# Kernel tuning notes

Hardware: AMD Instinct MI355X
Metric: run time of the kernel (lower is better)

Reference implementation:

```python
import jax, jax.numpy as jnp
import numpy as np

HEAD_DIM = 128
NUM_HEADS = 16
GROUP_SIZE = 8


def setup_inputs() -> dict:
    key = jax.random.key(0)
    k1, k2, k3 = jax.random.split(key, 3)
    B, T, K = 2, 2048, 2048
    query = jax.random.normal(k1, (B, T, NUM_HEADS * HEAD_DIM), dtype=jnp.float32)
    k_ = jax.random.normal(k2, (B, K, NUM_HEADS, HEAD_DIM), dtype=jnp.float32)
    v_ = jax.random.normal(k3, (B, K, NUM_HEADS, HEAD_DIM), dtype=jnp.float32)
    return {"query": query, "key": k_, "value": v_}


def reference(query, key, value):
    B, T, _ = query.shape
    g = GROUP_SIZE
    # (B, T//g, g, H, D)
    gq = query.reshape(B, T // g, g, NUM_HEADS, HEAD_DIM)
    scale = jnp.sqrt(jnp.asarray(HEAD_DIM, dtype=query.dtype))
    # scores: (B, T//g, g, H, K)
    scores = jnp.einsum('btghd,bkhd->btghk', gq, key) / scale
    attention = jax.nn.softmax(scores, axis=-1)
    out = jnp.einsum('btghk,bkhd->btghd', attention, value)
    return out.reshape(B, T, -1)
```

## Files before the change

### kernel.cpp

```cpp
#include <hip/hip_runtime.h>


#define T_   2048
#define KLEN 2048
#define H_   16
#define D_   128
#define BH_  32
#define NT_  (KLEN / 64)

typedef unsigned short u16;
typedef short bf16x8 __attribute__((ext_vector_type(8), may_alias));
typedef float f32x4 __attribute__((ext_vector_type(4)));
typedef float f32x8 __attribute__((ext_vector_type(8), may_alias));
typedef unsigned int u32a __attribute__((may_alias));
typedef u16 u16a __attribute__((may_alias));

__device__ __forceinline__ u16 f2bf(float f) {
    unsigned int u = __builtin_bit_cast(unsigned int, f);
    u += 0x7fffu + ((u >> 16) & 1u);
    return (u16)(u >> 16);
}
__device__ __forceinline__ unsigned int pk2(float a, float b) {
    unsigned int r;
    asm("v_cvt_pk_bf16_f32 %0, %1, %2" : "=v"(r) : "v"(a), "v"(b));
    return r;
}

__device__ __forceinline__ void async_cp16(const void* g, void* l) {
    __builtin_amdgcn_global_load_lds(
        (const __attribute__((address_space(1))) unsigned int*)g,
        (__attribute__((address_space(3))) unsigned int*)l, 16, 0, 0);
}

#define FR_ELEMS ((size_t)KLEN * D_)
#define WS_NEED  (2 * BH_ * FR_ELEMS * sizeof(u16))
#define PW_BYTES 2304
#define SM_BUF   32768
#define SM_TOTAL (2 * SM_BUF + 4 * PW_BYTES)

__global__ __launch_bounds__(256)
void prep_fused(const float* __restrict__ k_g, const float* __restrict__ v_g,
                u16* __restrict__ kf, u16* __restrict__ vf) {
    __shared__ __align__(16) unsigned char sm[16384];
    if (blockIdx.x < 4096) {
        const int id   = blockIdx.x * 256 + threadIdx.x;
        const int lane = id & 63;
        const int dc   = (id >> 6) & 3;
        const int kb   = (id >> 8) & 127;
        const int bh   = id >> 15;
        const int b = bh >> 4, h = bh & 15;
        const int c = lane & 15, quad = lane >> 4;
        const float* src = k_g + ((size_t)(b * KLEN + kb * 16 + c) * H_ + h) * D_
                               + dc * 32 + quad * 8;
        f32x8 v = *(const f32x8*)src;
        uint4 w;
        w.x = pk2(v[0], v[1]); w.y = pk2(v[2], v[3]);
        w.z = pk2(v[4], v[5]); w.w = pk2(v[6], v[7]);
        *(uint4*)(kf + (size_t)id * 8) = w;
    } else {
        const int bid  = blockIdx.x - 4096;
        const int kt64 = bid & 31;
        const int bh   = bid >> 5;
        const int b = bh >> 4, h = bh & 15;
        const float* vbase = v_g + ((size_t)b * KLEN * H_ + h) * D_;
        const int sc0 = threadIdx.x & 15;
        const int spr = threadIdx.x >> 4;
        #pragma unroll
        for (int rr = 0; rr < 2; ++rr) {
            const int r0 = 2 * (spr + 16 * rr);
            const float* vp = vbase + (size_t)(kt64 * 64 + r0) * (H_ * D_) + sc0 * 8;
            f32x8 va = *(const f32x8*)vp;
            f32x8 vb = *(const f32x8*)(vp + H_ * D_);
            const int g_hi = r0 >> 3;
            const int woff = (r0 & 7) * 2;
            #pragma unroll
            for (int j = 0; j < 8; ++j) {
                const int d = sc0 * 8 + j;
                const int g = g_hi ^ ((d ^ (d >> 3)) & 7);
                *(u32a*)(sm + d * 128 + g * 16 + woff) = pk2(va[j], vb[j]);
            }
        }
        __syncthreads();
        u16* obase = vf + (size_t)bh * FR_ELEMS;
        #pragma unroll
        for (int i = 0; i < 4; ++i) {
            const int gid  = threadIdx.x + 256 * i;
            const int lane = gid & 63;
            const int dt   = (gid >> 6) & 7;
            const int kgl  = gid >> 9;
            const int c = lane & 15, quad = lane >> 4;
            const int d  = dt * 16 + c;
            const int kl = kgl * 32 + quad * 8;
            const int g  = (kl >> 3) ^ ((d ^ (d >> 3)) & 7);
            uint4 w = *(const uint4*)(sm + d * 128 + g * 16);
            const int kg = kt64 * 2 + kgl;
            *(uint4*)(obase + ((size_t)(kg * 8 + dt) * 64 + lane) * 8) = w;
        }
    }
}


__global__ __launch_bounds__(256, 2)
void gqa_fa4(const float* __restrict__ q_g, const u16* __restrict__ kf,
             const u16* __restrict__ vf, float* __restrict__ o_g) {
    __shared__ __align__(16) unsigned char smem[SM_TOTAL];

    const int lane = threadIdx.x & 63;
    const int wave = threadIdx.x >> 6;
    const int c    = lane & 15;
    const int quad = lane >> 4;

    const int blk = blockIdx.x;
    const int bh  = (blk & 7) * 4 + (blk >> 8);
    const int qt  = (blk >> 3) & 31;
    const int b   = bh >> 4, h = bh & 15;

    const int q0 = qt * 64 + wave * 16;

    bf16x8 qf[4];
    {
        const float* qbase = q_g + (size_t)(b * T_ + q0 + c) * (H_ * D_) + h * D_ + quad * 8;
        #pragma unroll
        for (int dc = 0; dc < 4; ++dc) {
            f32x8 qv = *(const f32x8*)(qbase + dc * 32);
            uint4 w;
            w.x = pk2(qv[0], qv[1]); w.y = pk2(qv[2], qv[3]);
            w.z = pk2(qv[4], qv[5]); w.w = pk2(qv[6], qv[7]);
            qf[dc] = __builtin_bit_cast(bf16x8, w);
        }
    }

    const u16* KFb = kf + (size_t)bh * FR_ELEMS;
    const u16* VFb = vf + (size_t)bh * FR_ELEMS;

    f32x4 acc_o[8];
    #pragma unroll
    for (int dt = 0; dt < 8; ++dt) acc_o[dt] = (f32x4){0.f, 0.f, 0.f, 0.f};
    float l_i[4] = {0.f, 0.f, 0.f, 0.f};

    const float kexp = 0.12751744f;
    unsigned char* Pw = smem + 2 * SM_BUF + wave * PW_BYTES;

    auto stage = [&](int buf, int kt) {
        const u16* ksrc = KFb + (size_t)kt * 8192;
        const u16* vsrc = VFb + (size_t)kt * 8192;
        unsigned char* base = smem + buf * SM_BUF;
        #pragma unroll
        for (int j = 0; j < 8; ++j) {
            const int idx = wave * 8 + j;
            if (idx < 16)
                async_cp16(ksrc + idx * 512 + lane * 8, base + idx * 1024);
            else
                async_cp16(vsrc + (idx - 16) * 512 + lane * 8,
                           base + 16384 + (idx - 16) * 1024);
        }
    };

    stage(0, 0);
    __syncthreads();

    for (int kt = 0; kt < NT_; ++kt) {
        const int cur = kt & 1;
        if (kt + 1 < NT_) stage(cur ^ 1, kt + 1);

        const unsigned char* kbuf = smem + cur * SM_BUF;
        const unsigned char* vbuf = kbuf + 16384;

        f32x4 s[4];
        __builtin_amdgcn_s_setprio(1);
        #pragma unroll
        for (int nt = 0; nt < 4; ++nt) {
            s[nt] = (f32x4){0.f, 0.f, 0.f, 0.f};
            #pragma unroll
            for (int dc = 0; dc < 4; ++dc) {
                bf16x8 kfr = *(const bf16x8*)(kbuf + (nt * 4 + dc) * 1024 + lane * 16);
                s[nt] = __builtin_amdgcn_mfma_f32_16x16x32_bf16(qf[dc], kfr, s[nt], 0, 0, 0);
            }
        }
        __builtin_amdgcn_s_setprio(0);

        #pragma unroll
        for (int r = 0; r < 4; ++r) {
            const float p0 = exp2f(s[0][r] * kexp);
            const float p1 = exp2f(s[1][r] * kexp);
            const float p2 = exp2f(s[2][r] * kexp);
            const float p3 = exp2f(s[3][r] * kexp);
            l_i[r] += (p0 + p1) + (p2 + p3);
            const unsigned int u01 = pk2(p0, p1);
            const unsigned int u23 = pk2(p2, p3);
            u16a* row = (u16a*)(Pw + (quad * 4 + r) * 144);
            row[c]      = (u16)u01;
            row[16 + c] = (u16)(u01 >> 16);
            row[32 + c] = (u16)u23;
            row[48 + c] = (u16)(u23 >> 16);
        }

        __builtin_amdgcn_s_setprio(1);
        #pragma unroll
        for (int kc = 0; kc < 2; ++kc) {
            bf16x8 pf = *(const bf16x8*)(Pw + (c * 72 + kc * 32 + quad * 8) * 2);
            #pragma unroll
            for (int dt = 0; dt < 8; ++dt) {
                bf16x8 vfr = *(const bf16x8*)(vbuf + (kc * 8 + dt) * 1024 + lane * 16);
                acc_o[dt] = __builtin_amdgcn_mfma_f32_16x16x32_bf16(pf, vfr, acc_o[dt], 0, 0, 0);
            }
        }
        __builtin_amdgcn_s_setprio(0);

        __syncthreads();
    }

    #pragma unroll
    for (int r = 0; r < 4; ++r) {
        float t = l_i[r];
        t += __shfl_xor(t, 1);
        t += __shfl_xor(t, 2);
        t += __shfl_xor(t, 4);
        t += __shfl_xor(t, 8);
        const float inv = 1.f / t;
        const int qrow = q0 + quad * 4 + r;
        float* op = o_g + (size_t)(b * T_ + qrow) * (H_ * D_) + h * D_ + c;
        #pragma unroll
        for (int dt = 0; dt < 8; ++dt)
            op[dt * 16] = acc_o[dt][r] * inv;
    }
}


#define VT_BYTES 16384
#define KT_BYTES (64 * 136 * 2)

__global__ __launch_bounds__(256, 2)
void gqa_fa_v1(const float* __restrict__ q_g, const float* __restrict__ k_g,
               const float* __restrict__ v_g, float* __restrict__ o_g) {
    __shared__ __align__(16) unsigned char smem[VT_BYTES + KT_BYTES + 4 * PW_BYTES];
    unsigned char* VtB = smem;
    unsigned char* KtB = smem + VT_BYTES;
    const int lane = threadIdx.x & 63;
    const int wave = threadIdx.x >> 6;
    const int c    = lane & 15;
    const int quad = lane >> 4;
    const int qt = blockIdx.x & 31;
    const int bh = blockIdx.x >> 5;
    const int h  = bh & 15;
    const int b  = bh >> 4;
    const int q0 = qt * 64 + wave * 16;
    bf16x8 qf[4];
    {
        const float* qbase = q_g + (size_t)(b * T_ + q0 + c) * (H_ * D_) + h * D_ + quad * 8;
        #pragma unroll
        for (int dc = 0; dc < 4; ++dc) {
            f32x8 qv = *(const f32x8*)(qbase + dc * 32);
            uint4 w;
            w.x = pk2(qv[0], qv[1]); w.y = pk2(qv[2], qv[3]);
            w.z = pk2(qv[4], qv[5]); w.w = pk2(qv[6], qv[7]);
            qf[dc] = __builtin_bit_cast(bf16x8, w);
        }
    }
    f32x4 acc_o[8];
    #pragma unroll
    for (int dt = 0; dt < 8; ++dt) acc_o[dt] = (f32x4){0.f, 0.f, 0.f, 0.f};
    float m_i[4], l_i[4];
    #pragma unroll
    for (int r = 0; r < 4; ++r) { m_i[r] = -1e30f; l_i[r] = 0.f; }
    const float kexp = 0.12751744f;
    unsigned char* Pw = smem + VT_BYTES + KT_BYTES + wave * PW_BYTES;
    const int sc0 = threadIdx.x & 15;
    const int spr = threadIdx.x >> 4;
    const size_t kvstride = (size_t)(H_ * D_);
    const float* kbase = k_g + ((size_t)b * KLEN * H_ + h) * D_;
    const float* vbase = v_g + ((size_t)b * KLEN * H_ + h) * D_;
    for (int kt = 0; kt < KLEN / 64; ++kt) {
        __syncthreads();
        #pragma unroll
        for (int i = 0; i < 4; ++i) {
            const int id   = threadIdx.x + 256 * i;
            const int row  = id >> 4;
            const int dcol = (id & 15) * 8;
            const float* kp = kbase + (size_t)(kt * 64 + row) * kvstride + dcol;
            f32x8 kv = *(const f32x8*)kp;
            uint4 w;
            w.x = pk2(kv[0], kv[1]); w.y = pk2(kv[2], kv[3]);
            w.z = pk2(kv[4], kv[5]); w.w = pk2(kv[6], kv[7]);
            *(uint4*)(KtB + (row * 136 + dcol) * 2) = w;
        }
        #pragma unroll
        for (int rr = 0; rr < 2; ++rr) {
            const int r0 = 2 * (spr + 16 * rr);
            const float* vp = vbase + (size_t)(kt * 64 + r0) * kvstride + sc0 * 8;
            f32x8 va = *(const f32x8*)vp;
            f32x8 vb = *(const f32x8*)(vp + kvstride);
            const int g_hi = r0 >> 3;
            const int woff = (r0 & 7) * 2;
            #pragma unroll
            for (int j = 0; j < 8; ++j) {
                const int d = sc0 * 8 + j;
                const int g = g_hi ^ ((d ^ (d >> 3)) & 7);
                *(u32a*)(VtB + d * 128 + g * 16 + woff) = pk2(va[j], vb[j]);
            }
        }
        __syncthreads();
        f32x4 s[4];
        #pragma unroll
        for (int nt = 0; nt < 4; ++nt) {
            s[nt] = (f32x4){0.f, 0.f, 0.f, 0.f};
            const u16* kfp = (const u16*)KtB + (nt * 16 + c) * 136 + quad * 8;
            #pragma unroll
            for (int dc = 0; dc < 4; ++dc) {
                bf16x8 kfr = *(const bf16x8*)(kfp + dc * 32);
                s[nt] = __builtin_amdgcn_mfma_f32_16x16x32_bf16(qf[dc], kfr, s[nt], 0, 0, 0);
            }
        }
        #pragma unroll
        for (int r = 0; r < 4; ++r) {
            float v = fmaxf(fmaxf(s[0][r], s[1][r]), fmaxf(s[2][r], s[3][r]));
            v = fmaxf(v, __shfl_xor(v, 1));
            v = fmaxf(v, __shfl_xor(v, 2));
            v = fmaxf(v, __shfl_xor(v, 4));
            v = fmaxf(v, __shfl_xor(v, 8));
            const float mnew  = fmaxf(m_i[r], v);
            const float alpha = exp2f((m_i[r] - mnew) * kexp);
            m_i[r] = mnew;
            l_i[r] *= alpha;
            #pragma unroll
            for (int dt = 0; dt < 8; ++dt) acc_o[dt][r] *= alpha;
            float sum = 0.f;
            #pragma unroll
            for (int nt = 0; nt < 4; ++nt) {
                const float p = exp2f((s[nt][r] - mnew) * kexp);
                sum += p;
                *(u16a*)(Pw + ((quad * 4 + r) * 72 + nt * 16 + c) * 2) = f2bf(p);
            }
            float t = sum;
            t += __shfl_xor(t, 1);
            t += __shfl_xor(t, 2);
            t += __shfl_xor(t, 4);
            t += __shfl_xor(t, 8);
            l_i[r] += t;
        }
        __syncthreads();
        #pragma unroll
        for (int kc = 0; kc < 2; ++kc) {
            bf16x8 pf = *(const bf16x8*)(Pw + (c * 72 + kc * 32 + quad * 8) * 2);
            const int k0 = kc * 32 + quad * 8;
            #pragma unroll
            for (int dt = 0; dt < 8; ++dt) {
                const int d = dt * 16 + c;
                const int g = (k0 >> 3) ^ ((d ^ (d >> 3)) & 7);
                bf16x8 vfr = *(const bf16x8*)(VtB + d * 128 + g * 16);
                acc_o[dt] = __builtin_amdgcn_mfma_f32_16x16x32_bf16(pf, vfr, acc_o[dt], 0, 0, 0);
            }
        }
    }
    #pragma unroll
    for (int r = 0; r < 4; ++r) {
        const float inv = 1.f / l_i[r];
        const int qrow = q0 + quad * 4 + r;
        float* op = o_g + (size_t)(b * T_ + qrow) * (H_ * D_) + h * D_ + c;
        #pragma unroll
        for (int dt = 0; dt < 8; ++dt)
            op[dt * 16] = acc_o[dt][r] * inv;
    }
}

extern "C" void kernel_launch(void* const* d_in, const int* in_sizes, int n_in,
                              void* d_out, int out_size, void* d_ws, size_t ws_size,
                              hipStream_t stream) {
    const float* q = (const float*)d_in[0];
    const float* k = (const float*)d_in[1];
    const float* v = (const float*)d_in[2];
    float* o = (float*)d_out;
    if (ws_size >= WS_NEED) {
        u16* kfb = (u16*)d_ws;
        u16* vfb = kfb + (size_t)BH_ * FR_ELEMS;
        prep_fused<<<dim3(5120), dim3(256), 0, stream>>>(k, v, kfb, vfb);
        gqa_fa4<<<dim3(1024), dim3(256), 0, stream>>>(q, kfb, vfb, o);
    } else {
        gqa_fa_v1<<<dim3(1024), dim3(256), 0, stream>>>(q, k, v, o);
    }
}
```

Measured before the change: 237.2 us.

## Process two 16-row query tiles per wave to reuse K/V fragments

Each wave now handles 32 query rows (two MFMA M-tiles) instead of 16. Every K and V fragment read from LDS feeds two MFMAs, and each block covers 128 queries, so the grid is halved and K/V staging traffic per query drops by half. The P scratch buffer is enlarged and given an XOR swizzle to avoid LDS bank conflicts. The cost is more accumulator registers per wave, a larger LDS footprint, and only 512 blocks, which may limit occupancy and wave-level parallelism.

```diff
diff --git a/kernel.cpp b/kernel.cpp
--- a/kernel.cpp
+++ b/kernel.cpp
@@ -34,8 +34,8 @@
 
 #define FR_ELEMS ((size_t)KLEN * D_)
 #define WS_NEED  (2 * BH_ * FR_ELEMS * sizeof(u16))
-#define PW_BYTES 2304
 #define SM_BUF   32768
+#define PW_BYTES 4096
 #define SM_TOTAL (2 * SM_BUF + 4 * PW_BYTES)
 
 __global__ __launch_bounds__(256)
@@ -111,32 +111,36 @@
     const int quad = lane >> 4;
 
     const int blk = blockIdx.x;
-    const int bh  = (blk & 7) * 4 + (blk >> 8);
-    const int qt  = (blk >> 3) & 31;
+    const int bh  = (blk & 7) * 4 + (blk >> 7);
+    const int qt  = (blk >> 3) & 15;
     const int b   = bh >> 4, h = bh & 15;
 
-    const int q0 = qt * 64 + wave * 16;
-
-    bf16x8 qf[4];
-    {
-        const float* qbase = q_g + (size_t)(b * T_ + q0 + c) * (H_ * D_) + h * D_ + quad * 8;
+    const int q0 = qt * 128 + wave * 32;
+
+    bf16x8 qf[2][4];
+    #pragma unroll
+    for (int mt = 0; mt < 2; ++mt) {
+        const float* qbase = q_g + (size_t)(b * T_ + q0 + mt * 16 + c) * (H_ * D_)
+                                 + h * D_ + quad * 8;
         #pragma unroll
         for (int dc = 0; dc < 4; ++dc) {
             f32x8 qv = *(const f32x8*)(qbase + dc * 32);
             uint4 w;
             w.x = pk2(qv[0], qv[1]); w.y = pk2(qv[2], qv[3]);
             w.z = pk2(qv[4], qv[5]); w.w = pk2(qv[6], qv[7]);
-            qf[dc] = __builtin_bit_cast(bf16x8, w);
+            qf[mt][dc] = __builtin_bit_cast(bf16x8, w);
         }
     }
 
     const u16* KFb = kf + (size_t)bh * FR_ELEMS;
     const u16* VFb = vf + (size_t)bh * FR_ELEMS;
 
-    f32x4 acc_o[8];
-    #pragma unroll
-    for (int dt = 0; dt < 8; ++dt) acc_o[dt] = (f32x4){0.f, 0.f, 0.f, 0.f};
-    float l_i[4] = {0.f, 0.f, 0.f, 0.f};
+    f32x4 acc_o[2][8];
+    #pragma unroll
+    for (int mt = 0; mt < 2; ++mt)
+        #pragma unroll
+        for (int dt = 0; dt < 8; ++dt) acc_o[mt][dt] = (f32x4){0.f, 0.f, 0.f, 0.f};
+    float l_i[2][4] = {{0.f, 0.f, 0.f, 0.f}, {0.f, 0.f, 0.f, 0.f}};
 
     const float kexp = 0.12751744f;
     unsigned char* Pw = smem + 2 * SM_BUF + wave * PW_BYTES;
@@ -166,43 +170,56 @@
         const unsigned char* kbuf = smem + cur * SM_BUF;
         const unsigned char* vbuf = kbuf + 16384;
 
-        f32x4 s[4];
+        f32x4 s0[4], s1[4];
         __builtin_amdgcn_s_setprio(1);
         #pragma unroll
         for (int nt = 0; nt < 4; ++nt) {
-            s[nt] = (f32x4){0.f, 0.f, 0.f, 0.f};
+            s0[nt] = (f32x4){0.f, 0.f, 0.f, 0.f};
+            s1[nt] = (f32x4){0.f, 0.f, 0.f, 0.f};
             #pragma unroll
             for (int dc = 0; dc < 4; ++dc) {
                 bf16x8 kfr = *(const bf16x8*)(kbuf + (nt * 4 + dc) * 1024 + lane * 16);
-                s[nt] = __builtin_amdgcn_mfma_f32_16x16x32_bf16(qf[dc], kfr, s[nt], 0, 0, 0);
+                s0[nt] = __builtin_amdgcn_mfma_f32_16x16x32_bf16(qf[0][dc], kfr, s0[nt], 0, 0, 0);
+                s1[nt] = __builtin_amdgcn_mfma_f32_16x16x32_bf16(qf[1][dc], kfr, s1[nt], 0, 0, 0);
             }
         }
         __builtin_amdgcn_s_setprio(0);
 
         #pragma unroll
-        for (int r = 0; r < 4; ++r) {
-            const float p0 = exp2f(s[0][r] * kexp);
-            const float p1 = exp2f(s[1][r] * kexp);
-            const float p2 = exp2f(s[2][r] * kexp);
-            const float p3 = exp2f(s[3][r] * kexp);
-            l_i[r] += (p0 + p1) + (p2 + p3);
-            const unsigned int u01 = pk2(p0, p1);
-            const unsigned int u23 = pk2(p2, p3);
-            u16a* row = (u16a*)(Pw + (quad * 4 + r) * 144);
-            row[c]      = (u16)u01;
-            row[16 + c] = (u16)(u01 >> 16);
-            row[32 + c] = (u16)u23;
-            row[48 + c] = (u16)(u23 >> 16);
+        for (int mt = 0; mt < 2; ++mt) {
+            #pragma unroll
+            for (int r = 0; r < 4; ++r) {
+                const f32x4* s = mt ? s1 : s0;
+                const float p0 = exp2f(s[0][r] * kexp);
+                const float p1 = exp2f(s[1][r] * kexp);
+                const float p2 = exp2f(s[2][r] * kexp);
+                const float p3 = exp2f(s[3][r] * kexp);
+                l_i[mt][r] += (p0 + p1) + (p2 + p3);
+                const unsigned int u01 = pk2(p0, p1);
+                const unsigned int u23 = pk2(p2, p3);
+                const int prow = mt * 16 + quad * 4 + r;
+                unsigned char* row = Pw + prow * 128;
+                const int swz = (prow & 7) << 4;
+                *(u16a*)(row + ((2 * c) ^ swz))      = (u16)u01;
+                *(u16a*)(row + ((32 + 2 * c) ^ swz)) = (u16)(u01 >> 16);
+                *(u16a*)(row + ((64 + 2 * c) ^ swz)) = (u16)u23;
+                *(u16a*)(row + ((96 + 2 * c) ^ swz)) = (u16)(u23 >> 16);
+            }
         }
 
         __builtin_amdgcn_s_setprio(1);
         #pragma unroll
         for (int kc = 0; kc < 2; ++kc) {
-            bf16x8 pf = *(const bf16x8*)(Pw + (c * 72 + kc * 32 + quad * 8) * 2);
+            const int pr0 = c;
+            const int pr1 = 16 + c;
+            const int off = (kc * 64 + quad * 16) ^ ((c & 7) << 4);
+            bf16x8 pf0 = *(const bf16x8*)(Pw + pr0 * 128 + off);
+            bf16x8 pf1 = *(const bf16x8*)(Pw + pr1 * 128 + off);
             #pragma unroll
             for (int dt = 0; dt < 8; ++dt) {
                 bf16x8 vfr = *(const bf16x8*)(vbuf + (kc * 8 + dt) * 1024 + lane * 16);
-                acc_o[dt] = __builtin_amdgcn_mfma_f32_16x16x32_bf16(pf, vfr, acc_o[dt], 0, 0, 0);
+                acc_o[0][dt] = __builtin_amdgcn_mfma_f32_16x16x32_bf16(pf0, vfr, acc_o[0][dt], 0, 0, 0);
+                acc_o[1][dt] = __builtin_amdgcn_mfma_f32_16x16x32_bf16(pf1, vfr, acc_o[1][dt], 0, 0, 0);
             }
         }
         __builtin_amdgcn_s_setprio(0);
@@ -211,29 +228,33 @@
     }
 
     #pragma unroll
-    for (int r = 0; r < 4; ++r) {
-        float t = l_i[r];
-        t += __shfl_xor(t, 1);
-        t += __shfl_xor(t, 2);
-        t += __shfl_xor(t, 4);
-        t += __shfl_xor(t, 8);
-        const float inv = 1.f / t;
-        const int qrow = q0 + quad * 4 + r;
-        float* op = o_g + (size_t)(b * T_ + qrow) * (H_ * D_) + h * D_ + c;
-        #pragma unroll
-        for (int dt = 0; dt < 8; ++dt)
-            op[dt * 16] = acc_o[dt][r] * inv;
+    for (int mt = 0; mt < 2; ++mt) {
+        #pragma unroll
+        for (int r = 0; r < 4; ++r) {
+            float t = l_i[mt][r];
+            t += __shfl_xor(t, 1);
+            t += __shfl_xor(t, 2);
+            t += __shfl_xor(t, 4);
+            t += __shfl_xor(t, 8);
+            const float inv = 1.f / t;
+            const int qrow = q0 + mt * 16 + quad * 4 + r;
+            float* op = o_g + (size_t)(b * T_ + qrow) * (H_ * D_) + h * D_ + c;
+            #pragma unroll
+            for (int dt = 0; dt < 8; ++dt)
+                op[dt * 16] = acc_o[mt][dt][r] * inv;
+        }
     }
 }
 
 
 #define VT_BYTES 16384
 #define KT_BYTES (64 * 136 * 2)
+#define PWF_BYTES 2304
 
 __global__ __launch_bounds__(256, 2)
 void gqa_fa_v1(const float* __restrict__ q_g, const float* __restrict__ k_g,
                const float* __restrict__ v_g, float* __restrict__ o_g) {
-    __shared__ __align__(16) unsigned char smem[VT_BYTES + KT_BYTES + 4 * PW_BYTES];
+    __shared__ __align__(16) unsigned char smem[VT_BYTES + KT_BYTES + 4 * PWF_BYTES];
     unsigned char* VtB = smem;
     unsigned char* KtB = smem + VT_BYTES;
     const int lane = threadIdx.x & 63;
@@ -264,7 +285,7 @@
     #pragma unroll
     for (int r = 0; r < 4; ++r) { m_i[r] = -1e30f; l_i[r] = 0.f; }
     const float kexp = 0.12751744f;
-    unsigned char* Pw = smem + VT_BYTES + KT_BYTES + wave * PW_BYTES;
+    unsigned char* Pw = smem + VT_BYTES + KT_BYTES + wave * PWF_BYTES;
     const int sc0 = threadIdx.x & 15;
     const int spr = threadIdx.x >> 4;
     const size_t kvstride = (size_t)(H_ * D_);
@@ -374,7 +395,7 @@
         u16* kfb = (u16*)d_ws;
         u16* vfb = kfb + (size_t)BH_ * FR_ELEMS;
         prep_fused<<<dim3(5120), dim3(256), 0, stream>>>(k, v, kfb, vfb);
-        gqa_fa4<<<dim3(1024), dim3(256), 0, stream>>>(q, kfb, vfb, o);
+        gqa_fa4<<<dim3(512), dim3(256), 0, stream>>>(q, kfb, vfb, o);
     } else {
         gqa_fa_v1<<<dim3(1024), dim3(256), 0, stream>>>(q, k, v, o);
     }
```

Measured after the change: 222.0 us. 6.4% less time.

## Switch attention to 32x32x16 MFMA with register-resident P via permlane swap

Applied to the files above, without the earlier changes.

Rewrites the fast attention kernel to use 32x32x16 bf16 MFMAs with 8 waves of 32 query rows each (256 queries per block), and changes the K/V pre-pack layout in the prep kernel to match the new fragment shapes. S is computed transposed (K as A operand), so the softmax probabilities can be repacked into the PV A-operand in registers using v_permlane32_swap instead of a round trip through LDS. The goal is fewer LDS writes and reads, fewer MFMA issues, and more reuse of each K/V tile across queries. In exchange it raises register pressure (f32x16 accumulators, 8 Q fragments) and launches only 256 blocks, which may leave some compute units underused.

```diff
diff --git a/kernel.cpp b/kernel.cpp
--- a/kernel.cpp
+++ b/kernel.cpp
@@ -12,6 +12,7 @@
 typedef short bf16x8 __attribute__((ext_vector_type(8), may_alias));
 typedef float f32x4 __attribute__((ext_vector_type(4)));
 typedef float f32x8 __attribute__((ext_vector_type(8), may_alias));
+typedef float f32x16 __attribute__((ext_vector_type(16)));
 typedef unsigned int u32a __attribute__((may_alias));
 typedef u16 u16a __attribute__((may_alias));
 
@@ -25,6 +26,9 @@
     asm("v_cvt_pk_bf16_f32 %0, %1, %2" : "=v"(r) : "v"(a), "v"(b));
     return r;
 }
+__device__ __forceinline__ void pl_swap(unsigned int& a, unsigned int& b) {
+    asm("v_permlane32_swap_b32 %0, %1" : "+v"(a), "+v"(b));
+}
 
 __device__ __forceinline__ void async_cp16(const void* g, void* l) {
     __builtin_amdgcn_global_load_lds(
@@ -34,24 +38,23 @@
 
 #define FR_ELEMS ((size_t)KLEN * D_)
 #define WS_NEED  (2 * BH_ * FR_ELEMS * sizeof(u16))
-#define PW_BYTES 2304
 #define SM_BUF   32768
-#define SM_TOTAL (2 * SM_BUF + 4 * PW_BYTES)
 
 __global__ __launch_bounds__(256)
 void prep_fused(const float* __restrict__ k_g, const float* __restrict__ v_g,
                 u16* __restrict__ kf, u16* __restrict__ vf) {
     __shared__ __align__(16) unsigned char sm[16384];
     if (blockIdx.x < 4096) {
-        const int id   = blockIdx.x * 256 + threadIdx.x;
-        const int lane = id & 63;
-        const int dc   = (id >> 6) & 3;
-        const int kb   = (id >> 8) & 127;
-        const int bh   = id >> 15;
+        const int id     = blockIdx.x * 256 + threadIdx.x;
+        const int lane   = id & 63;
+        const int dchunk = (id >> 6) & 7;
+        const int ktile  = (id >> 9) & 1;
+        const int kt64   = (id >> 10) & 31;
+        const int bh     = id >> 15;
         const int b = bh >> 4, h = bh & 15;
-        const int c = lane & 15, quad = lane >> 4;
-        const float* src = k_g + ((size_t)(b * KLEN + kb * 16 + c) * H_ + h) * D_
-                               + dc * 32 + quad * 8;
+        const int key = kt64 * 64 + ktile * 32 + (lane & 31);
+        const int d0  = dchunk * 16 + (lane >> 5) * 8;
+        const float* src = k_g + ((size_t)(b * KLEN + key) * H_ + h) * D_ + d0;
         f32x8 v = *(const f32x8*)src;
         uint4 w;
         w.x = pk2(v[0], v[1]); w.y = pk2(v[2], v[3]);
@@ -84,70 +87,87 @@
         u16* obase = vf + (size_t)bh * FR_ELEMS;
         #pragma unroll
         for (int i = 0; i < 4; ++i) {
-            const int gid  = threadIdx.x + 256 * i;
-            const int lane = gid & 63;
-            const int dt   = (gid >> 6) & 7;
-            const int kgl  = gid >> 9;
-            const int c = lane & 15, quad = lane >> 4;
-            const int d  = dt * 16 + c;
-            const int kl = kgl * 32 + quad * 8;
-            const int g  = (kl >> 3) ^ ((d ^ (d >> 3)) & 7);
+            const int gid   = threadIdx.x + 256 * i;
+            const int lane  = gid & 63;
+            const int ntile = (gid >> 6) & 3;
+            const int kc    = (gid >> 8) & 3;
+            const int key0  = kc * 16 + (lane >> 5) * 8;
+            const int d     = ntile * 32 + (lane & 31);
+            const int g     = (key0 >> 3) ^ ((d ^ (d >> 3)) & 7);
             uint4 w = *(const uint4*)(sm + d * 128 + g * 16);
-            const int kg = kt64 * 2 + kgl;
-            *(uint4*)(obase + ((size_t)(kg * 8 + dt) * 64 + lane) * 8) = w;
-        }
-    }
-}
-
-
-__global__ __launch_bounds__(256, 2)
-void gqa_fa4(const float* __restrict__ q_g, const u16* __restrict__ kf,
+            *(uint4*)(obase + ((size_t)(kt64 * 16 + kc * 4 + ntile) * 64 + lane) * 8) = w;
+        }
+    }
+}
+
+
+struct PA2 { bf16x8 f0, f1; };
+
+__device__ __forceinline__ PA2 softmax_pack(f32x16 st, float kexp, float& lacc) {
+    float p[16];
+    #pragma unroll
+    for (int r = 0; r < 16; ++r) p[r] = exp2f(st[r] * kexp);
+    lacc += (((p[0] + p[1]) + (p[2] + p[3])) + ((p[4] + p[5]) + (p[6] + p[7])))
+          + (((p[8] + p[9]) + (p[10] + p[11])) + ((p[12] + p[13]) + (p[14] + p[15])));
+    unsigned int a0 = pk2(p[0], p[1]),   b0 = pk2(p[4], p[5]);
+    unsigned int a1 = pk2(p[2], p[3]),   b1 = pk2(p[6], p[7]);
+    unsigned int a2 = pk2(p[8], p[9]),   b2 = pk2(p[12], p[13]);
+    unsigned int a3 = pk2(p[10], p[11]), b3 = pk2(p[14], p[15]);
+    pl_swap(a0, b0); pl_swap(a1, b1); pl_swap(a2, b2); pl_swap(a3, b3);
+    uint4 w0; w0.x = a0; w0.y = a1; w0.z = b0; w0.w = b1;
+    uint4 w1; w1.x = a2; w1.y = a3; w1.z = b2; w1.w = b3;
+    PA2 r;
+    r.f0 = __builtin_bit_cast(bf16x8, w0);
+    r.f1 = __builtin_bit_cast(bf16x8, w1);
+    return r;
+}
+
+__global__ __launch_bounds__(512, 2)
+void gqa_fa5(const float* __restrict__ q_g, const u16* __restrict__ kf,
              const u16* __restrict__ vf, float* __restrict__ o_g) {
-    __shared__ __align__(16) unsigned char smem[SM_TOTAL];
+    __shared__ __align__(16) unsigned char smem[2 * SM_BUF];
 
     const int lane = threadIdx.x & 63;
     const int wave = threadIdx.x >> 6;
-    const int c    = lane & 15;
-    const int quad = lane >> 4;
+    const int half = lane >> 5;
+    const int col  = lane & 31;
 
     const int blk = blockIdx.x;
-    const int bh  = (blk & 7) * 4 + (blk >> 8);
-    const int qt  = (blk >> 3) & 31;
-    const int b   = bh >> 4, h = bh & 15;
-
-    const int q0 = qt * 64 + wave * 16;
-
-    bf16x8 qf[4];
+    const int bh  = (blk & 7) * 4 + (blk >> 6);
+    const int qt  = (blk >> 3) & 7;
+    const int b = bh >> 4, h = bh & 15;
+
+    const int q0 = qt * 256 + wave * 32;
+
+    bf16x8 qf[8];
     {
-        const float* qbase = q_g + (size_t)(b * T_ + q0 + c) * (H_ * D_) + h * D_ + quad * 8;
-        #pragma unroll
-        for (int dc = 0; dc < 4; ++dc) {
-            f32x8 qv = *(const f32x8*)(qbase + dc * 32);
+        const float* qbase = q_g + (size_t)(b * T_ + q0 + col) * (H_ * D_)
+                                 + h * D_ + half * 8;
+        #pragma unroll
+        for (int dchunk = 0; dchunk < 8; ++dchunk) {
+            f32x8 qv = *(const f32x8*)(qbase + dchunk * 16);
             uint4 w;
             w.x = pk2(qv[0], qv[1]); w.y = pk2(qv[2], qv[3]);
             w.z = pk2(qv[4], qv[5]); w.w = pk2(qv[6], qv[7]);
-            qf[dc] = __builtin_bit_cast(bf16x8, w);
+            qf[dchunk] = __builtin_bit_cast(bf16x8, w);
         }
     }
 
     const u16* KFb = kf + (size_t)bh * FR_ELEMS;
     const u16* VFb = vf + (size_t)bh * FR_ELEMS;
 
-    f32x4 acc_o[8];
-    #pragma unroll
-    for (int dt = 0; dt < 8; ++dt) acc_o[dt] = (f32x4){0.f, 0.f, 0.f, 0.f};
-    float l_i[4] = {0.f, 0.f, 0.f, 0.f};
+    f32x16 acc[4] = {};
+    float l_part = 0.f;
 
     const float kexp = 0.12751744f;
-    unsigned char* Pw = smem + 2 * SM_BUF + wave * PW_BYTES;
 
     auto stage = [&](int buf, int kt) {
         const u16* ksrc = KFb + (size_t)kt * 8192;
         const u16* vsrc = VFb + (size_t)kt * 8192;
         unsigned char* base = smem + buf * SM_BUF;
         #pragma unroll
-        for (int j = 0; j < 8; ++j) {
-            const int idx = wave * 8 + j;
+        for (int j = 0; j < 4; ++j) {
+            const int idx = wave * 4 + j;
             if (idx < 16)
                 async_cp16(ksrc + idx * 512 + lane * 8, base + idx * 1024);
             else
@@ -166,43 +186,31 @@
         const unsigned char* kbuf = smem + cur * SM_BUF;
         const unsigned char* vbuf = kbuf + 16384;
 
-        f32x4 s[4];
+        f32x16 s0 = {}, s1 = {};
         __builtin_amdgcn_s_setprio(1);
         #pragma unroll
-        for (int nt = 0; nt < 4; ++nt) {
-            s[nt] = (f32x4){0.f, 0.f, 0.f, 0.f};
-            #pragma unroll
-            for (int dc = 0; dc < 4; ++dc) {
-                bf16x8 kfr = *(const bf16x8*)(kbuf + (nt * 4 + dc) * 1024 + lane * 16);
-                s[nt] = __builtin_amdgcn_mfma_f32_16x16x32_bf16(qf[dc], kfr, s[nt], 0, 0, 0);
-            }
+        for (int dchunk = 0; dchunk < 8; ++dchunk) {
+            bf16x8 kfr0 = *(const bf16x8*)(kbuf + dchunk * 1024 + lane * 16);
+            bf16x8 kfr1 = *(const bf16x8*)(kbuf + (8 + dchunk) * 1024 + lane * 16);
+            s0 = __builtin_amdgcn_mfma_f32_32x32x16_bf16(kfr0, qf[dchunk], s0, 0, 0, 0);
+            s1 = __builtin_amdgcn_mfma_f32_32x32x16_bf16(kfr1, qf[dchunk], s1, 0, 0, 0);
         }
         __builtin_amdgcn_s_setprio(0);
 
-        #pragma unroll
-        for (int r = 0; r < 4; ++r) {
-            const float p0 = exp2f(s[0][r] * kexp);
-            const float p1 = exp2f(s[1][r] * kexp);
-            const float p2 = exp2f(s[2][r] * kexp);
-            const float p3 = exp2f(s[3][r] * kexp);
-            l_i[r] += (p0 + p1) + (p2 + p3);
-            const unsigned int u01 = pk2(p0, p1);
-            const unsigned int u23 = pk2(p2, p3);
-            u16a* row = (u16a*)(Pw + (quad * 4 + r) * 144);
-            row[c]      = (u16)u01;
-            row[16 + c] = (u16)(u01 >> 16);
-            row[32 + c] = (u16)u23;
-            row[48 + c] = (u16)(u23 >> 16);
-        }
-
+        PA2 pa01 = softmax_pack(s0, kexp, l_part);
+        PA2 pa23 = softmax_pack(s1, kexp, l_part);
+
+        bf16x8 pfrag0 = pa01.f0, pfrag1 = pa01.f1;
+        bf16x8 pfrag2 = pa23.f0, pfrag3 = pa23.f1;
         __builtin_amdgcn_s_setprio(1);
         #pragma unroll
-        for (int kc = 0; kc < 2; ++kc) {
-            bf16x8 pf = *(const bf16x8*)(Pw + (c * 72 + kc * 32 + quad * 8) * 2);
-            #pragma unroll
-            for (int dt = 0; dt < 8; ++dt) {
-                bf16x8 vfr = *(const bf16x8*)(vbuf + (kc * 8 + dt) * 1024 + lane * 16);
-                acc_o[dt] = __builtin_amdgcn_mfma_f32_16x16x32_bf16(pf, vfr, acc_o[dt], 0, 0, 0);
+        for (int kc = 0; kc < 4; ++kc) {
+            const bf16x8 paf = (kc == 0) ? pfrag0 : (kc == 1) ? pfrag1
+                             : (kc == 2) ? pfrag2 : pfrag3;
+            #pragma unroll
+            for (int nt2 = 0; nt2 < 4; ++nt2) {
+                bf16x8 vfr = *(const bf16x8*)(vbuf + (kc * 4 + nt2) * 1024 + lane * 16);
+                acc[nt2] = __builtin_amdgcn_mfma_f32_32x32x16_bf16(paf, vfr, acc[nt2], 0, 0, 0);
             }
         }
         __builtin_amdgcn_s_setprio(0);
@@ -210,30 +218,30 @@
         __syncthreads();
     }
 
-    #pragma unroll
-    for (int r = 0; r < 4; ++r) {
-        float t = l_i[r];
-        t += __shfl_xor(t, 1);
-        t += __shfl_xor(t, 2);
-        t += __shfl_xor(t, 4);
-        t += __shfl_xor(t, 8);
-        const float inv = 1.f / t;
-        const int qrow = q0 + quad * 4 + r;
-        float* op = o_g + (size_t)(b * T_ + qrow) * (H_ * D_) + h * D_ + c;
-        #pragma unroll
-        for (int dt = 0; dt < 8; ++dt)
-            op[dt * 16] = acc_o[dt][r] * inv;
+    const float l_full = l_part + __shfl_xor(l_part, 32);
+    float* lds_l = (float*)smem;
+    if (half == 0) lds_l[wave * 32 + col] = 1.f / l_full;
+    __syncthreads();
+    #pragma unroll
+    for (int r = 0; r < 16; ++r) {
+        const int qrow = (r & 3) + 8 * (r >> 2) + 4 * half;
+        const float inv = lds_l[wave * 32 + qrow];
+        float* op = o_g + (size_t)(b * T_ + q0 + qrow) * (H_ * D_) + h * D_ + col;
+        #pragma unroll
+        for (int nt2 = 0; nt2 < 4; ++nt2)
+            op[nt2 * 32] = acc[nt2][r] * inv;
     }
 }
 
 
 #define VT_BYTES 16384
 #define KT_BYTES (64 * 136 * 2)
+#define PWF_BYTES 2304
 
 __global__ __launch_bounds__(256, 2)
 void gqa_fa_v1(const float* __restrict__ q_g, const float* __restrict__ k_g,
                const float* __restrict__ v_g, float* __restrict__ o_g) {
-    __shared__ __align__(16) unsigned char smem[VT_BYTES + KT_BYTES + 4 * PW_BYTES];
+    __shared__ __align__(16) unsigned char smem[VT_BYTES + KT_BYTES + 4 * PWF_BYTES];
     unsigned char* VtB = smem;
     unsigned char* KtB = smem + VT_BYTES;
     const int lane = threadIdx.x & 63;
@@ -264,7 +272,7 @@
     #pragma unroll
     for (int r = 0; r < 4; ++r) { m_i[r] = -1e30f; l_i[r] = 0.f; }
     const float kexp = 0.12751744f;
-    unsigned char* Pw = smem + VT_BYTES + KT_BYTES + wave * PW_BYTES;
+    unsigned char* Pw = smem + VT_BYTES + KT_BYTES + wave * PWF_BYTES;
     const int sc0 = threadIdx.x & 15;
     const int spr = threadIdx.x >> 4;
     const size_t kvstride = (size_t)(H_ * D_);
@@ -374,7 +382,7 @@
         u16* kfb = (u16*)d_ws;
         u16* vfb = kfb + (size_t)BH_ * FR_ELEMS;
         prep_fused<<<dim3(5120), dim3(256), 0, stream>>>(k, v, kfb, vfb);
-        gqa_fa4<<<dim3(1024), dim3(256), 0, stream>>>(q, kfb, vfb, o);
+        gqa_fa5<<<dim3(256), dim3(512), 0, stream>>>(q, kfb, vfb, o);
     } else {
         gqa_fa_v1<<<dim3(1024), dim3(256), 0, stream>>>(q, k, v, o);
     }
```

New measurement: 206.1 us. 1.15x faster.
